# Kernel optimization log

Measured on AMD Instinct MI355X. Metric: run time of the kernel, lower is better.

Reference implementation:

```python
import jax, jax.numpy as jnp
import numpy as np

B, T, D = 128, 197, 768          # batch, tokens, model dim
HEADS, HID_PER_HEAD = 12, 64
H = HEADS * HID_PER_HEAD         # lstm hidden size (== D by construction)


def _block_mask(in_per_head, hid_per_head, head_num):
    """Block-diagonal mask replicated over the 4 LSTM gates (i,f,g,o)."""
    Ht = hid_per_head * head_num
    Dt = in_per_head * head_num
    m = np.zeros((4 * Ht, Dt), np.float32)
    for h in range(head_num):
        for g in range(4):
            r0 = g * Ht + h * hid_per_head
            m[r0:r0 + hid_per_head, h * in_per_head:(h + 1) * in_per_head] = 1.0
    return jnp.asarray(m)


def setup_inputs() -> dict:
    key = jax.random.key(0)
    ks = jax.random.split(key, 16)
    s = 1.0 / np.sqrt(H)  # pytorch LSTM init scale
    u = lambda k, shape: jax.random.uniform(k, shape, jnp.float32, -s, s)
    mask_ih = _block_mask(D // HEADS, HID_PER_HEAD, HEADS)   # [4H, D]
    mask_hh = _block_mask(HID_PER_HEAD, HID_PER_HEAD, HEADS)  # [4H, H]
    inp = {
        "x": jax.random.normal(ks[0], (B, T, D), jnp.float32),
        "pre_w": u(ks[1], (D, D)),
        "pre_b": u(ks[2], (D,)),
        "w_ih_f": u(ks[3], (4 * H, D)) * mask_ih,
        "w_hh_f": u(ks[4], (4 * H, H)) * mask_hh,
        "b_ih_f": u(ks[5], (4 * H,)),
        "b_hh_f": u(ks[6], (4 * H,)),
        "w_ih_r": u(ks[7], (4 * H, D)) * mask_ih,
        "w_hh_r": u(ks[8], (4 * H, H)) * mask_hh,
        "b_ih_r": u(ks[9], (4 * H,)),
        "b_hh_r": u(ks[10], (4 * H,)),
        "proj_w": u(ks[11], (D, 2 * H)),
        "proj_b": u(ks[12], (D,)),
    }
    return inp


def _lstm_dir(x, w_ih, w_hh, b_ih, b_hh, reverse):
    # Precompute input contribution for all timesteps: [B,T,4H]
    xg = jnp.einsum('btd,gd->btg', x, w_ih) + b_ih + b_hh
    xs = jnp.swapaxes(xg, 0, 1)  # [T,B,4H]
    Bn = x.shape[0]

    def step(carry, gx):
        h, c = carry
        gates = gx + h @ w_hh.T
        i, f, g, o = jnp.split(gates, 4, axis=-1)  # pytorch gate order i,f,g,o
        i = jax.nn.sigmoid(i)
        f = jax.nn.sigmoid(f)
        g = jnp.tanh(g)
        o = jax.nn.sigmoid(o)
        c = f * c + i * g
        h = o * jnp.tanh(c)
        return (h, c), h

    init = (jnp.zeros((Bn, w_hh.shape[1]), x.dtype),
            jnp.zeros((Bn, w_hh.shape[1]), x.dtype))
    _, hs = jax.lax.scan(step, init, xs, reverse=reverse)  # outputs aligned to input order
    return jnp.swapaxes(hs, 0, 1)  # [B,T,H]


def reference(x, pre_w, pre_b, w_ih_f, w_hh_f, b_ih_f, b_hh_f,
              w_ih_r, w_hh_r, b_ih_r, b_hh_r, proj_w, proj_b):
    x = x @ pre_w.T + pre_b                      # pre_proj
    hf = _lstm_dir(x, w_ih_f, w_hh_f, b_ih_f, b_hh_f, reverse=False)
    hr = _lstm_dir(x, w_ih_r, w_hh_r, b_ih_r, b_hh_r, reverse=True)
    lstm_out = jnp.concatenate([hf, hr], axis=-1)  # [B,T,2H]
    return lstm_out @ proj_w.T + proj_b            # proj -> [B,T,D]
```

## Files before the change

kernel.cpp:

```cpp
#include <hip/hip_runtime.h>
#include <stdint.h>


#define DEV __device__ __forceinline__

typedef __attribute__((ext_vector_type(8))) short short8;
typedef __attribute__((ext_vector_type(4))) float floatx4;

#define BATCH 128
#define TT    197
#define DD    768
#define NH    12
#define NROWS (BATCH*TT)
#define G4H   3072
#define MT    197
#define NT    6

DEV uint16_t f2bf(float f) {
    union { float f; uint32_t u; } v; v.f = f;
    uint32_t r = (v.u + 0x7FFF + ((v.u >> 16) & 1)) >> 16;
    return (uint16_t)r;
}

DEV floatx4 mfma16(short8 a, short8 b, floatx4 c) {
    return __builtin_amdgcn_mfma_f32_16x16x32_bf16(a, b, c, 0, 0, 0);
}

DEV float sigf(float x)   { return __builtin_amdgcn_rcpf(1.0f + __expf(-x)); }
DEV float tanhf_(float x) { return 1.0f - 2.0f * __builtin_amdgcn_rcpf(1.0f + __expf(2.0f * x)); }

DEV void async16(const uint16_t* g, uint16_t* l) {
    __builtin_amdgcn_global_load_lds(
        (const __attribute__((address_space(1))) unsigned int*)g,
        (__attribute__((address_space(3))) unsigned int*)l,
        16, 0, 0);
}

#define CFENCE() asm volatile("" ::: "memory")
#define WAITCNT_LGKM0_ONLY 0xC07F
#define WAITCNT_VM4        0x0F74
#define WAITCNT_VM0        0x0F70

struct CvtArgs {
    const float* src[7];
    uint16_t*    dst[7];
    int          n4[7];
    int          nseg;
};

__global__ void cvt_multi(CvtArgs a) {
    int tid = blockIdx.x * blockDim.x + threadIdx.x;
    int stride = gridDim.x * blockDim.x;
    for (int s = 0; s < a.nseg; s++) {
        const float4* src = (const float4*)a.src[s];
        ushort4* dst = (ushort4*)a.dst[s];
        int n4 = a.n4[s];
        for (int i = tid; i < n4; i += stride) {
            float4 v = src[i];
            ushort4 o;
            o.x = f2bf(v.x); o.y = f2bf(v.y); o.z = f2bf(v.z); o.w = f2bf(v.w);
            dst[i] = o;
        }
    }
}

template<int STORE_BF16, int LAYOUT>
__global__ __launch_bounds__(256, 4) void gemm128p(
    const uint16_t* __restrict__ A,
    const uint16_t* __restrict__ Bw,
    const float*    __restrict__ bias,
    void*           __restrict__ C,
    int K, int Ntot)
{
    __shared__ __attribute__((aligned(16))) uint16_t As[2][4096];
    __shared__ __attribute__((aligned(16))) uint16_t Bs[2][4096];

    const int bid = blockIdx.x;
    const int c   = bid & 7;
    const int j   = bid >> 3;
    const int mt_ = c + 8 * (j / NT);
    const int nt_ = j % NT;
    if (mt_ >= MT) return;
    const int m0 = mt_ * 128;
    const int n0 = nt_ * 128;

    const int tid  = threadIdx.x;
    const int wv   = tid >> 6;
    const int lane = tid & 63;
    const int ln   = lane & 15;
    const int q    = lane >> 4;
    const int wm   = wv >> 1;
    const int wn   = wv & 1;

    floatx4 acc[4][4];
#pragma unroll
    for (int a = 0; a < 4; a++)
#pragma unroll
        for (int b = 0; b < 4; b++) acc[a][b] = (floatx4){0.f, 0.f, 0.f, 0.f};

    const uint32_t oA0 = (uint32_t)(m0 + (2*wv+0)*16 + ln) * (uint32_t)K + q*8;
    const uint32_t oA1 = (uint32_t)(m0 + (2*wv+1)*16 + ln) * (uint32_t)K + q*8;
    const uint32_t oB0 = (uint32_t)(n0 + (2*wv+0)*16 + ln) * (uint32_t)K + q*8;
    const uint32_t oB1 = (uint32_t)(n0 + (2*wv+1)*16 + ln) * (uint32_t)K + q*8;

    const int NI = K >> 5;

    auto stage = [&](int kiter) {
        const int buf = kiter & 1;
        uint32_t k0 = (uint32_t)(kiter * 32);
        if (k0 >= (uint32_t)K) k0 = 0;
        async16(A  + oA0 + k0, &As[buf][(2*wv+0)*512]);
        async16(A  + oA1 + k0, &As[buf][(2*wv+1)*512]);
        async16(Bw + oB0 + k0, &Bs[buf][(2*wv+0)*512]);
        async16(Bw + oB1 + k0, &Bs[buf][(2*wv+1)*512]);
    };

    stage(0);

    for (int i = 0; i < NI; i += 2) {
#pragma unroll
        for (int u = 0; u < 2; u++) {
            stage(i + u + 1);
            CFENCE();
            __builtin_amdgcn_s_waitcnt(WAITCNT_VM4);
            __builtin_amdgcn_s_barrier();
            CFENCE();

            short8 af[4];
#pragma unroll
            for (int mt = 0; mt < 4; mt++)
                af[mt] = *(const short8*)&As[u][(wm*4 + mt)*512 + lane*8];
#pragma unroll
            for (int nt = 0; nt < 4; nt++) {
                short8 bf = *(const short8*)&Bs[u][(wn*4 + nt)*512 + lane*8];
#pragma unroll
                for (int mt = 0; mt < 4; mt++)
                    acc[mt][nt] = mfma16(af[mt], bf, acc[mt][nt]);
            }

            CFENCE();
            __builtin_amdgcn_s_barrier();
            CFENCE();
        }
    }
    __builtin_amdgcn_s_waitcnt(WAITCNT_VM0);

#pragma unroll
    for (int mt = 0; mt < 4; mt++)
#pragma unroll
        for (int nt = 0; nt < 4; nt++) {
            int n = n0 + (wn*4 + nt)*16 + ln;
            float bv = bias[n];
#pragma unroll
            for (int r = 0; r < 4; r++) {
                int m = m0 + (wm*4 + mt)*16 + q*4 + r;
                float val = acc[mt][nt][r] + bv;
                if (LAYOUT == 1) {
                    int b = m / 197; int t = m - b*197;
                    int head = n >> 6; int d = n & 63;
                    size_t off = ((size_t)(t*NH + head)*BATCH + b)*64 + d;
                    ((uint16_t*)C)[off] = f2bf(val);
                } else {
                    size_t off = (size_t)m * Ntot + n;
                    if (STORE_BF16) ((uint16_t*)C)[off] = f2bf(val);
                    else            ((float*)C)[off]    = val;
                }
            }
        }
}

__global__ __launch_bounds__(256) void lstm_fused(
    const uint16_t* __restrict__ pre,
    const uint16_t* __restrict__ wih_f, const uint16_t* __restrict__ whh_f,
    const uint16_t* __restrict__ wih_r, const uint16_t* __restrict__ whh_r,
    const float* __restrict__ bih_f, const float* __restrict__ bhh_f,
    const float* __restrict__ bih_r, const float* __restrict__ bhh_r,
    uint16_t* __restrict__ hout)
{
    __shared__ __attribute__((aligned(16))) uint16_t hbuf[2][16][72];

    const int tid  = threadIdx.x;
    const int wv   = tid >> 6;
    const int lane = tid & 63;
    const int ln   = lane & 15;
    const int q    = lane >> 4;
    const int b0   = blockIdx.x * 16;
    const int head = blockIdx.y;
    const int dir  = blockIdx.z;
    const int ub   = wv * 16;

    const uint16_t* wih = dir ? wih_r : wih_f;
    const uint16_t* whh = dir ? whh_r : whh_f;
    const float*    bih = dir ? bih_r : bih_f;
    const float*    bhh = dir ? bhh_r : bhh_f;

    short8 aih[4][2], ahh[4][2];
#pragma unroll
    for (int t = 0; t < 4; t++) {
        size_t row = (size_t)(t*768 + head*64 + ub + ln);
#pragma unroll
        for (int s = 0; s < 2; s++) {
            aih[t][s] = *(const short8*)(wih + row*768 + head*64 + s*32 + q*8);
            ahh[t][s] = *(const short8*)(whh + row*768 + head*64 + s*32 + q*8);
        }
    }
    float biasv[4][4];
#pragma unroll
    for (int t = 0; t < 4; t++)
#pragma unroll
        for (int r = 0; r < 4; r++) {
            int row = t*768 + head*64 + ub + q*4 + r;
            biasv[t][r] = bih[row] + bhh[row];
        }

    for (int i = tid; i < 2*16*72; i += 256) ((uint16_t*)hbuf)[i] = 0;
    float c[4] = {0.f, 0.f, 0.f, 0.f};
    __syncthreads();

    const uint16_t* xbase = pre + (size_t)head*BATCH*64 + (size_t)(b0 + ln)*64 + q*8;
    uint16_t* hw = hout + ((size_t)(b0 + ln)*TT)*1536 + dir*768 + head*64 + ub + q*4;

    int t_cur = dir ? (TT - 1) : 0;
    const int tstep = dir ? -1 : 1;
    size_t xo = (size_t)t_cur * NH * BATCH * 64;
    short8 xv0 = *(const short8*)(xbase + xo);
    short8 xv1 = *(const short8*)(xbase + xo + 32);

    for (int step = 0; step < TT; step++) {
        short8 cx0 = xv0, cx1 = xv1;
        int t_next = t_cur + tstep;
        if (step + 1 < TT) {
            size_t xo2 = (size_t)t_next * NH * BATCH * 64;
            xv0 = *(const short8*)(xbase + xo2);
            xv1 = *(const short8*)(xbase + xo2 + 32);
        }
        const int pb = (step + 1) & 1;
        const int cb = step & 1;
        short8 hb0 = *(const short8*)&hbuf[pb][ln][0*32 + q*8];
        short8 hb1 = *(const short8*)&hbuf[pb][ln][1*32 + q*8];

        floatx4 acc[4];
#pragma unroll
        for (int t = 0; t < 4; t++)
            acc[t] = (floatx4){biasv[t][0], biasv[t][1], biasv[t][2], biasv[t][3]};
#pragma unroll
        for (int t = 0; t < 4; t++) {
            acc[t] = mfma16(aih[t][0], cx0, acc[t]);
            acc[t] = mfma16(ahh[t][0], hb0, acc[t]);
            acc[t] = mfma16(aih[t][1], cx1, acc[t]);
            acc[t] = mfma16(ahh[t][1], hb1, acc[t]);
        }

        float hv[4];
#pragma unroll
        for (int r = 0; r < 4; r++) {
            float ig = sigf(acc[0][r]);
            float fg = sigf(acc[1][r]);
            float gg = tanhf_(acc[2][r]);
            float og = sigf(acc[3][r]);
            c[r] = fg * c[r] + ig * gg;
            hv[r] = og * tanhf_(c[r]);
        }
        uint2 hp;
        asm volatile("v_cvt_pk_bf16_f32 %0, %1, %2" : "=v"(hp.x) : "v"(hv[0]), "v"(hv[1]));
        asm volatile("v_cvt_pk_bf16_f32 %0, %1, %2" : "=v"(hp.y) : "v"(hv[2]), "v"(hv[3]));

        *(uint2*)&hbuf[cb][ln][ub + q*4] = hp;
        *(uint2*)(hw + (size_t)t_cur * 1536) = hp;

        CFENCE();
        __builtin_amdgcn_s_waitcnt(WAITCNT_LGKM0_ONLY);
        __builtin_amdgcn_s_barrier();
        CFENCE();

        t_cur = t_next;
    }
}

extern "C" void kernel_launch(void* const* d_in, const int* in_sizes, int n_in,
                              void* d_out, int out_size, void* d_ws, size_t ws_size,
                              hipStream_t stream) {
    (void)in_sizes; (void)n_in; (void)out_size; (void)ws_size;
    const float* x     = (const float*)d_in[0];
    const float* pre_w = (const float*)d_in[1];
    const float* pre_b = (const float*)d_in[2];
    const float* wihf  = (const float*)d_in[3];
    const float* whhf  = (const float*)d_in[4];
    const float* bihf  = (const float*)d_in[5];
    const float* bhhf  = (const float*)d_in[6];
    const float* wihr  = (const float*)d_in[7];
    const float* whhr  = (const float*)d_in[8];
    const float* bihr  = (const float*)d_in[9];
    const float* bhhr  = (const float*)d_in[10];
    const float* projw = (const float*)d_in[11];
    const float* projb = (const float*)d_in[12];
    float* out = (float*)d_out;

    uint16_t* W = (uint16_t*)d_ws;
    uint16_t* xb     = W; W += (size_t)NROWS * DD;
    uint16_t* bwpre  = W; W += (size_t)DD * DD;
    uint16_t* bwihf  = W; W += (size_t)G4H * DD;
    uint16_t* bwhhf  = W; W += (size_t)G4H * DD;
    uint16_t* bwihr  = W; W += (size_t)G4H * DD;
    uint16_t* bwhhr  = W; W += (size_t)G4H * DD;
    uint16_t* bwproj = W; W += (size_t)DD * 2 * DD;
    uint16_t* preb   = W; W += (size_t)NROWS * DD;
    uint16_t* houtb  = W; W += (size_t)NROWS * 2 * DD;

    CvtArgs ca;
    ca.src[0] = x;     ca.dst[0] = xb;     ca.n4[0] = (int)((size_t)NROWS * DD / 4);
    ca.src[1] = pre_w; ca.dst[1] = bwpre;  ca.n4[1] = DD * DD / 4;
    ca.src[2] = wihf;  ca.dst[2] = bwihf;  ca.n4[2] = G4H * DD / 4;
    ca.src[3] = whhf;  ca.dst[3] = bwhhf;  ca.n4[3] = G4H * DD / 4;
    ca.src[4] = wihr;  ca.dst[4] = bwihr;  ca.n4[4] = G4H * DD / 4;
    ca.src[5] = whhr;  ca.dst[5] = bwhhr;  ca.n4[5] = G4H * DD / 4;
    ca.src[6] = projw; ca.dst[6] = bwproj; ca.n4[6] = DD * 2 * DD / 4;
    ca.nseg = 7;
    hipLaunchKernelGGL(cvt_multi, dim3(1024), dim3(256), 0, stream, ca);

    const int RPX = (MT + 7) / 8;
    const int GBLK = 8 * RPX * NT;

    hipLaunchKernelGGL((gemm128p<1, 1>), dim3(GBLK), dim3(256), 0, stream,
                       xb, bwpre, pre_b, (void*)preb, DD, DD);
    hipLaunchKernelGGL(lstm_fused, dim3(8, 12, 2), dim3(256), 0, stream,
                       preb, bwihf, bwhhf, bwihr, bwhhr,
                       bihf, bhhf, bihr, bhhr, houtb);
    hipLaunchKernelGGL((gemm128p<0, 0>), dim3(GBLK), dim3(256), 0, stream,
                       houtb, bwproj, projb, (void*)out, 2 * DD, DD);
}
```

Before: 487.0 us.

## Replace 128x128 GEMM with 256x256 eight-wave ping-pong pipelined kernel

The pre-projection and output-projection GEMMs move from 128x128 tiles with 4 waves to 256x256 tiles with 8 waves and 128KB LDS, using a K-step of 64. Loads for the next tiles are interleaved with four MFMA quadrants under s_setprio, and a contiguous XCD-aware block swizzle is added. The aim is higher arithmetic intensity and better overlap of global loads with MFMA. The costs are lower occupancy, row clamping and masking for the partial last M tile, and many more barriers per K step.

Result: slower. 524.7 us (+7.7%).

```diff
diff --git a/kernel.cpp b/kernel.cpp
--- a/kernel.cpp
+++ b/kernel.cpp
@@ -13,8 +13,8 @@
 #define NH    12
 #define NROWS (BATCH*TT)
 #define G4H   3072
-#define MT    197
-#define NT    6
+#define MT8   99
+#define NT8   3
 
 DEV uint16_t f2bf(float f) {
     union { float f; uint32_t u; } v; v.f = f;
@@ -64,106 +64,156 @@
     }
 }
 
+#define PH_BAR() do { CFENCE(); __builtin_amdgcn_s_barrier(); CFENCE(); } while(0)
+
+#define MFMA_QUAD(QM, QN) do { \
+    __builtin_amdgcn_s_setprio(1); \
+    _Pragma("unroll") \
+    for (int ii = 0; ii < 4; ii++) \
+        _Pragma("unroll") \
+        for (int j = 0; j < 2; j++) { \
+            acc[(QM)*4+ii][(QN)*2+j] = mfma16(af[ii][0], bfr[QN][j][0], acc[(QM)*4+ii][(QN)*2+j]); \
+            acc[(QM)*4+ii][(QN)*2+j] = mfma16(af[ii][1], bfr[QN][j][1], acc[(QM)*4+ii][(QN)*2+j]); \
+        } \
+    __builtin_amdgcn_s_setprio(0); \
+} while(0)
+
 template<int STORE_BF16, int LAYOUT>
-__global__ __launch_bounds__(256, 4) void gemm128p(
+__global__ __launch_bounds__(512, 2) void gemm256q(
     const uint16_t* __restrict__ A,
     const uint16_t* __restrict__ Bw,
     const float*    __restrict__ bias,
     void*           __restrict__ C,
     int K, int Ntot)
 {
-    __shared__ __attribute__((aligned(16))) uint16_t As[2][4096];
-    __shared__ __attribute__((aligned(16))) uint16_t Bs[2][4096];
-
-    const int bid = blockIdx.x;
-    const int c   = bid & 7;
-    const int j   = bid >> 3;
-    const int mt_ = c + 8 * (j / NT);
-    const int nt_ = j % NT;
-    if (mt_ >= MT) return;
-    const int m0 = mt_ * 128;
-    const int n0 = nt_ * 128;
+    __shared__ __attribute__((aligned(16))) uint16_t lds[65536];
+
+    const int nwg = gridDim.x;
+    const int qq = nwg >> 3, rr = nwg & 7;
+    const int xcd = blockIdx.x & 7, loc = blockIdx.x >> 3;
+    const int swz = (xcd < rr ? xcd*(qq+1) : rr*(qq+1) + (xcd-rr)*qq) + loc;
+    const int mt_ = swz / NT8, nt_ = swz - mt_*NT8;
+    const int m0 = mt_*256, n0 = nt_*256;
 
     const int tid  = threadIdx.x;
     const int wv   = tid >> 6;
     const int lane = tid & 63;
     const int ln   = lane & 15;
     const int q    = lane >> 4;
-    const int wm   = wv >> 1;
-    const int wn   = wv & 1;
-
-    floatx4 acc[4][4];
-#pragma unroll
-    for (int a = 0; a < 4; a++)
-#pragma unroll
-        for (int b = 0; b < 4; b++) acc[a][b] = (floatx4){0.f, 0.f, 0.f, 0.f};
-
-    const uint32_t oA0 = (uint32_t)(m0 + (2*wv+0)*16 + ln) * (uint32_t)K + q*8;
-    const uint32_t oA1 = (uint32_t)(m0 + (2*wv+1)*16 + ln) * (uint32_t)K + q*8;
-    const uint32_t oB0 = (uint32_t)(n0 + (2*wv+0)*16 + ln) * (uint32_t)K + q*8;
-    const uint32_t oB1 = (uint32_t)(n0 + (2*wv+1)*16 + ln) * (uint32_t)K + q*8;
-
-    const int NI = K >> 5;
-
-    auto stage = [&](int kiter) {
-        const int buf = kiter & 1;
-        uint32_t k0 = (uint32_t)(kiter * 32);
-        if (k0 >= (uint32_t)K) k0 = 0;
-        async16(A  + oA0 + k0, &As[buf][(2*wv+0)*512]);
-        async16(A  + oA1 + k0, &As[buf][(2*wv+1)*512]);
-        async16(Bw + oB0 + k0, &Bs[buf][(2*wv+0)*512]);
-        async16(Bw + oB1 + k0, &Bs[buf][(2*wv+1)*512]);
+    const int wm   = wv >> 2;
+    const int wnx  = wv & 3;
+    const int NKT  = K >> 6;
+
+    floatx4 acc[8][4];
+#pragma unroll
+    for (int i = 0; i < 8; i++)
+#pragma unroll
+        for (int j = 0; j < 4; j++) acc[i][j] = (floatx4){0.f, 0.f, 0.f, 0.f};
+
+    const int c0   = wv * 2;
+    const int rsub = lane >> 3;
+    const int kq8  = (lane & 7) * 8;
+    uint32_t gA[2][2], gB[2][2];
+#pragma unroll
+    for (int h = 0; h < 2; h++)
+#pragma unroll
+        for (int l = 0; l < 2; l++) {
+            int row = m0 + h*128 + (c0 + l)*8 + rsub;
+            if (row >= NROWS) row = NROWS - 1;
+            gA[h][l] = (uint32_t)row * (uint32_t)K + kq8;
+            gB[h][l] = (uint32_t)(n0 + h*128 + (c0 + l)*8 + rsub) * (uint32_t)K + kq8;
+        }
+
+    const int aL = (wm*128 + ln)*64 + q*8;
+    const int bL = 32768 + wnx*4096 + ln*64 + q*8;
+
+    auto stA = [&](int kt, int h) {
+        uint32_t k0 = (kt < NKT) ? (uint32_t)(kt << 6) : 0u;
+        uint16_t* d = &lds[(kt & 1)*16384 + h*8192 + c0*512];
+        async16(A + gA[h][0] + k0, d);
+        async16(A + gA[h][1] + k0, d + 512);
     };
-
-    stage(0);
-
-    for (int i = 0; i < NI; i += 2) {
-#pragma unroll
-        for (int u = 0; u < 2; u++) {
-            stage(i + u + 1);
-            CFENCE();
-            __builtin_amdgcn_s_waitcnt(WAITCNT_VM4);
-            __builtin_amdgcn_s_barrier();
-            CFENCE();
-
-            short8 af[4];
-#pragma unroll
-            for (int mt = 0; mt < 4; mt++)
-                af[mt] = *(const short8*)&As[u][(wm*4 + mt)*512 + lane*8];
-#pragma unroll
-            for (int nt = 0; nt < 4; nt++) {
-                short8 bf = *(const short8*)&Bs[u][(wn*4 + nt)*512 + lane*8];
-#pragma unroll
-                for (int mt = 0; mt < 4; mt++)
-                    acc[mt][nt] = mfma16(af[mt], bf, acc[mt][nt]);
-            }
-
-            CFENCE();
-            __builtin_amdgcn_s_barrier();
-            CFENCE();
-        }
+    auto stB = [&](int kt, int h) {
+        uint32_t k0 = (kt < NKT) ? (uint32_t)(kt << 6) : 0u;
+        uint16_t* d = &lds[32768 + (kt & 1)*16384 + h*8192 + c0*512];
+        async16(Bw + gB[h][0] + k0, d);
+        async16(Bw + gB[h][1] + k0, d + 512);
+    };
+
+    stB(0,0); stB(0,1); stA(0,0); stA(0,1); stB(1,0); stB(1,1);
+    CFENCE();
+    __builtin_amdgcn_s_waitcnt(WAITCNT_VM4);
+    __builtin_amdgcn_s_barrier();
+    CFENCE();
+
+    short8 af[4][2];
+    short8 bfr[2][2][2];
+
+    for (int tt = 0; tt < NKT; tt++) {
+        const int lb = (tt & 1) * 16384;
+#pragma unroll
+        for (int ii = 0; ii < 4; ii++) {
+            af[ii][0] = *(const short8*)&lds[lb + aL + ii*1024];
+            af[ii][1] = *(const short8*)&lds[lb + aL + ii*1024 + 32];
+        }
+#pragma unroll
+        for (int j = 0; j < 2; j++) {
+            bfr[0][j][0] = *(const short8*)&lds[lb + bL + j*1024];
+            bfr[0][j][1] = *(const short8*)&lds[lb + bL + j*1024 + 32];
+        }
+        stA(tt + 1, 0);
+        PH_BAR();
+        MFMA_QUAD(0, 0);
+        PH_BAR();
+#pragma unroll
+        for (int j = 0; j < 2; j++) {
+            bfr[1][j][0] = *(const short8*)&lds[lb + bL + (2+j)*1024];
+            bfr[1][j][1] = *(const short8*)&lds[lb + bL + (2+j)*1024 + 32];
+        }
+        stA(tt + 1, 1);
+        PH_BAR();
+        MFMA_QUAD(0, 1);
+        PH_BAR();
+#pragma unroll
+        for (int ii = 0; ii < 4; ii++) {
+            af[ii][0] = *(const short8*)&lds[lb + aL + (4+ii)*1024];
+            af[ii][1] = *(const short8*)&lds[lb + aL + (4+ii)*1024 + 32];
+        }
+        stB(tt + 2, 0);
+        PH_BAR();
+        MFMA_QUAD(1, 0);
+        PH_BAR();
+        stB(tt + 2, 1);
+        CFENCE();
+        __builtin_amdgcn_s_waitcnt(WAITCNT_VM4);
+        __builtin_amdgcn_s_barrier();
+        CFENCE();
+        MFMA_QUAD(1, 1);
+        PH_BAR();
     }
     __builtin_amdgcn_s_waitcnt(WAITCNT_VM0);
 
 #pragma unroll
-    for (int mt = 0; mt < 4; mt++)
-#pragma unroll
-        for (int nt = 0; nt < 4; nt++) {
-            int n = n0 + (wn*4 + nt)*16 + ln;
+    for (int i = 0; i < 8; i++)
+#pragma unroll
+        for (int jj = 0; jj < 4; jj++) {
+            int n = n0 + wnx*64 + jj*16 + ln;
             float bv = bias[n];
 #pragma unroll
             for (int r = 0; r < 4; r++) {
-                int m = m0 + (wm*4 + mt)*16 + q*4 + r;
-                float val = acc[mt][nt][r] + bv;
-                if (LAYOUT == 1) {
-                    int b = m / 197; int t = m - b*197;
-                    int head = n >> 6; int d = n & 63;
-                    size_t off = ((size_t)(t*NH + head)*BATCH + b)*64 + d;
-                    ((uint16_t*)C)[off] = f2bf(val);
-                } else {
-                    size_t off = (size_t)m * Ntot + n;
-                    if (STORE_BF16) ((uint16_t*)C)[off] = f2bf(val);
-                    else            ((float*)C)[off]    = val;
+                int m = m0 + wm*128 + i*16 + q*4 + r;
+                if (m < NROWS) {
+                    float val = acc[i][jj][r] + bv;
+                    if (LAYOUT == 1) {
+                        int b = m / 197; int t = m - b*197;
+                        int head = n >> 6; int d = n & 63;
+                        size_t off = ((size_t)(t*NH + head)*BATCH + b)*64 + d;
+                        ((uint16_t*)C)[off] = f2bf(val);
+                    } else {
+                        size_t off = (size_t)m * Ntot + n;
+                        if (STORE_BF16) ((uint16_t*)C)[off] = f2bf(val);
+                        else            ((float*)C)[off]    = val;
+                    }
                 }
             }
         }
@@ -318,14 +368,13 @@
     ca.nseg = 7;
     hipLaunchKernelGGL(cvt_multi, dim3(1024), dim3(256), 0, stream, ca);
 
-    const int RPX = (MT + 7) / 8;
-    const int GBLK = 8 * RPX * NT;
-
-    hipLaunchKernelGGL((gemm128p<1, 1>), dim3(GBLK), dim3(256), 0, stream,
+    const int GBLK8 = MT8 * NT8;
+
+    hipLaunchKernelGGL((gemm256q<1, 1>), dim3(GBLK8), dim3(512), 0, stream,
                        xb, bwpre, pre_b, (void*)preb, DD, DD);
     hipLaunchKernelGGL(lstm_fused, dim3(8, 12, 2), dim3(256), 0, stream,
                        preb, bwihf, bwhhf, bwihr, bwhhr,
                        bihf, bhhf, bihr, bhhr, houtb);
-    hipLaunchKernelGGL((gemm128p<0, 0>), dim3(GBLK), dim3(256), 0, stream,
+    hipLaunchKernelGGL((gemm256q<0, 0>), dim3(GBLK8), dim3(512), 0, stream,
                        houtb, bwproj, projb, (void*)out, 2 * DD, DD);
 }
```
